# Optimization experiments

Hardware: AMD Instinct MI355X
Metric: run time of the kernel (lower is better)

The kernel has to match this reference:

```python
import jax, jax.numpy as jnp
import numpy as np
from jax.scipy.special import logsumexp

G, H, L, N, K = 2000, 128, 10, 4096, 10
TAU, LC, LA, EPS = 0.1, 1.0, 0.5, 1e-6

def _lin_init(k, fi, fo):
    return jax.random.normal(k, (fi, fo), jnp.float32) / np.sqrt(fi)

def setup_inputs():
    key = jax.random.key(0)
    ks = jax.random.split(key, 12)
    return {
        'wt_x': jax.random.normal(ks[0], (N, G), jnp.float32),
        'ko_x': jax.random.normal(ks[1], (N, G), jnp.float32),
        'wt_labels': jax.random.randint(ks[2], (N,), 0, K, dtype=jnp.int32),
        'ko_labels': jax.random.randint(ks[3], (N,), 0, K, dtype=jnp.int32),
        'enc_w1': _lin_init(ks[4], G, H), 'enc_b1': jnp.zeros((H,)),
        'enc_g': jnp.ones((H,)), 'enc_be': jnp.zeros((H,)),
        'enc_w2': _lin_init(ks[5], H, L), 'enc_b2': jnp.zeros((L,)),
        'kap_w1': _lin_init(ks[6], G, H), 'kap_b1': jnp.zeros((H,)),
        'kap_g': jnp.ones((H,)), 'kap_be': jnp.zeros((H,)),
        'kap_w2': _lin_init(ks[7], H, 1), 'kap_b2': jnp.zeros((1,)),
        'dec_w1': _lin_init(ks[8], L, H), 'dec_b1': jnp.zeros((H,)),
        'dec_g': jnp.ones((H,)), 'dec_be': jnp.zeros((H,)),
        'dec_w2': _lin_init(ks[9], H, G), 'dec_b2': jnp.zeros((G,)),
    }

def _mlp(x, w1, b1, g, be, w2, b2):
    # Linear -> LayerNorm -> ReLU -> Linear (dropout_prob=0)
    h = x @ w1 + b1
    m = h.mean(-1, keepdims=True)
    v = ((h - m) ** 2).mean(-1, keepdims=True)
    h = (h - m) / jnp.sqrt(v + 1e-5) * g + be
    return jax.nn.relu(h) @ w2 + b2

def _contrastive(z_wt, z_ko, y_wt, y_ko):
    S = (z_wt @ z_ko.T) / TAU  # [Nwt, Nko], unit-norm z so |S| <= 1/tau
    total = jnp.float32(0.0)
    n_shared = jnp.float32(0.0)
    for c in range(K):  # fixed small class count
        mwt = (y_wt == c).astype(S.dtype)
        mko = (y_ko == c).astype(S.dtype)
        n_wt, n_ko = mwt.sum(), mko.sum()
        valid = (n_wt > 0) & (n_ko > 0)
        nw, nk = jnp.maximum(n_wt, 1.0), jnp.maximum(n_ko, 1.0)
        # mean_{i in c, j in c} (LSE_i - S_ij) over ko columns of class c
        lse_r = logsumexp(jnp.where(mko[None, :] > 0, S, -1e4), axis=1)
        l1 = jnp.sum(mwt * (lse_r - (S @ mko) / nk)) / nw
        lse_c = logsumexp(jnp.where(mwt[:, None] > 0, S, -1e4), axis=0)
        l2 = jnp.sum(mko * (lse_c - (mwt @ S) / nw)) / nk
        total = total + jnp.where(valid, 0.5 * (l1 + l2), 0.0)
        n_shared = n_shared + valid.astype(S.dtype)
    return jnp.where(n_shared > 0, total / jnp.maximum(n_shared, 1.0), 0.0)

def _alignment(z, y):
    ones = jnp.ones(z.shape[0], z.dtype)
    counts = jax.ops.segment_sum(ones, y, num_segments=K)
    mu_c = jax.ops.segment_sum(z, y, num_segments=K) / jnp.maximum(counts, 1.0)[:, None]
    dev = z - mu_c[y]
    per_class = jax.ops.segment_sum(jnp.sum(dev ** 2, axis=1), y, num_segments=K) / jnp.maximum(counts, 1.0)
    present = counts > 0
    return jnp.sum(jnp.where(present, per_class, 0.0)) / jnp.maximum(jnp.sum(present.astype(z.dtype)), 1.0)

def reference(wt_x, ko_x, enc_w1, enc_b1, enc_g, enc_be, enc_w2, enc_b2, kap_w1, kap_b1, kap_g, kap_be, kap_w2, kap_b2, dec_w1, dec_b1, dec_g, dec_be, dec_w2, dec_b2, wt_labels, ko_labels):
    def encode(x):
        mu = _mlp(x, enc_w1, enc_b1, enc_g, enc_be, enc_w2, enc_b2)
        mu = mu / jnp.maximum(jnp.linalg.norm(mu, axis=1, keepdims=True), 1e-12)
        kappa = jax.nn.softplus(_mlp(x, kap_w1, kap_b1, kap_g, kap_be, kap_w2, kap_b2)) + EPS
        return mu, kappa
    wt_mu, wt_kappa = encode(wt_x)
    ko_mu, ko_kappa = encode(ko_x)
    wt_z, ko_z = wt_mu, ko_mu  # eval mode: z = mu (deterministic)
    wt_rec = _mlp(wt_z, dec_w1, dec_b1, dec_g, dec_be, dec_w2, dec_b2)
    ko_rec = _mlp(ko_z, dec_w1, dec_b1, dec_g, dec_be, dec_w2, dec_b2)
    recon = jnp.mean((wt_rec - wt_x) ** 2) + jnp.mean((ko_rec - ko_x) ** 2)
    kl = (wt_kappa.mean() + ko_kappa.mean()) * 0.01
    contrast = _contrastive(wt_z, ko_z, wt_labels, ko_labels)
    align = _alignment(jnp.concatenate([wt_z, ko_z], 0), jnp.concatenate([wt_labels, ko_labels], 0))
    return recon + kl + LC * contrast + LA * align
```

## Files before the change

### kernel.cpp

```cpp
#include <hip/hip_runtime.h>
#include <math.h>

typedef __attribute__((ext_vector_type(8))) __bf16 bf16x8;
typedef __attribute__((ext_vector_type(4))) float f32x4;

#define GL2LDS_(gptr, lptr) \
    __builtin_amdgcn_global_load_lds((const __attribute__((address_space(1))) void*)(gptr), \
                                     (__attribute__((address_space(3))) void*)(lptr), 16, 0, 0)

#define OFF_NWT   0
#define OFF_NKO   10
#define OFF_L1    20
#define OFF_L2    30
#define OFF_REC   162
#define IOFF_WTOFF 192
#define IOFF_KOOFF 204
#define IOFF_WTCTR 216
#define ACC_FLOATS 256

#define WT_OFF    256
#define WTLO_OFF  (WT_OFF + 262144)
#define H_OFF     (WTLO_OFF + 262144)
#define Z_OFF     (H_OFF + 2097152)
#define KAP_OFF   (Z_OFF + 81920)
#define HREST_OFF (KAP_OFF + 8192)
#define HPART     2097152

__global__ __launch_bounds__(256) void pack_w_kernel(const float* __restrict__ enc_w1,
                                                     const float* __restrict__ kap_w1,
                                                     __bf16* __restrict__ WThi,
                                                     __bf16* __restrict__ WTlo)
{
    __shared__ float tile[64][65];
    int kt = blockIdx.x & 31;
    int ct = blockIdx.x >> 5;
    int k0 = kt * 64, c0 = ct * 64;
    int t = threadIdx.x;
    int lr = t >> 6, lc = t & 63;
#pragma unroll
    for (int i = 0; i < 16; ++i) {
        int k = k0 + lr + 4 * i;
        int c = c0 + lc;
        float v = 0.f;
        if (k < 2000) v = (c < 128) ? enc_w1[(size_t)k * 128 + c]
                                    : kap_w1[(size_t)k * 128 + (c - 128)];
        tile[lc][lr + 4 * i] = v;
    }
    __syncthreads();
#pragma unroll
    for (int i = 0; i < 16; ++i) {
        int c = c0 + lr + 4 * i;
        int k = k0 + lc;
        float v = tile[lr + 4 * i][lc];
        __bf16 h = (__bf16)v;
        __bf16 l = (__bf16)(v - (float)h);
        size_t idx = (size_t)c * 2048 + k;
        WThi[idx] = h;
        WTlo[idx] = l;
    }
}

__global__ __launch_bounds__(256) void pack_dw2_kernel(const float* __restrict__ dw2,
                                                       __bf16* __restrict__ BThi,
                                                       __bf16* __restrict__ BTlo)
{
    __shared__ float tile[64][129];
    int j0 = blockIdx.x * 64;
    int t = threadIdx.x;
#pragma unroll
    for (int i = 0; i < 32; ++i) {
        int idx = i * 256 + t;
        int c = idx >> 6, jj = idx & 63;
        int j = j0 + jj;
        tile[jj][c] = (j < 2000) ? dw2[(size_t)c * 2000 + j] : 0.f;
    }
    __syncthreads();
#pragma unroll
    for (int i = 0; i < 32; ++i) {
        int idx = i * 256 + t;
        int jj = idx >> 7, c = idx & 127;
        float v = tile[jj][c];
        __bf16 h = (__bf16)v;
        size_t o = (size_t)(j0 + jj) * 128 + c;
        BThi[o] = h;
        BTlo[o] = (__bf16)(v - (float)h);
    }
}

__global__ void counts_kernel(const int* __restrict__ wtl, const int* __restrict__ kol,
                              float* __restrict__ acc)
{
    __shared__ int cw[10], ck[10];
    int t = threadIdx.x;
    if (t < 10) { cw[t] = 0; ck[t] = 0; }
    __syncthreads();
    for (int i = t; i < 4096; i += 1024) {
        atomicAdd(&cw[wtl[i]], 1);
        atomicAdd(&ck[kol[i]], 1);
    }
    __syncthreads();
    if (t < 10) { acc[OFF_NWT + t] = (float)cw[t]; acc[OFF_NKO + t] = (float)ck[t]; }
    if (t == 0) {
        int* ai = (int*)acc;
        int aw = 0, ak = 0;
        for (int c = 0; c < 10; ++c) {
            ai[IOFF_WTOFF + c] = aw; aw += cw[c];
            ai[IOFF_KOOFF + c] = ak; ak += ck[c];
        }
        ai[IOFF_WTOFF + 10] = aw;
        ai[IOFF_KOOFF + 10] = ak;
    }
}

__global__ __launch_bounds__(512) void gemm1_kernel(const float* __restrict__ wt_x,
                                                    const float* __restrict__ ko_x,
                                                    const __bf16* __restrict__ WThi,
                                                    const __bf16* __restrict__ WTlo,
                                                    float* __restrict__ Hb,
                                                    float* __restrict__ Hrest,
                                                    int nkc)
{
    __shared__ short Bs[2][2][2][4096];
    int t = threadIdx.x;
    int widx = t >> 6, lane = t & 63;
    int wm = widx >> 1, wn = widx & 1;
    int b = blockIdx.x;
    int mt = b & 63, strip = (b >> 6) & 1, kc = b >> 7;
    int R0 = mt * 128;
    int cb = strip * 128;
    int kchunk = 2048 / nkc;
    int kbase = kc * kchunk;
    int kleft = 2000 - kbase;
    int nsteps = (kleft < kchunk) ? ((kleft + 31) >> 5) : (kchunk >> 5);
    int ntiles = (nsteps + 1) >> 1;

    const float* xb = (R0 < 4096) ? (wt_x + (size_t)R0 * 2000)
                                  : (ko_x + (size_t)(R0 - 4096) * 2000);
    int ar = wm * 32 + (lane & 15);
    const float* xrow0 = xb + (size_t)ar * 2000 + kbase;
    const float* xrow1 = xrow0 + (size_t)16 * 2000;
    int kboff = (lane >> 4) * 8;

    int col0 = t >> 2;
    int s0   = (t & 3) ^ ((col0 >> 1) & 3);
    size_t boff = (size_t)(cb + col0) * 2048 + kbase + s0 * 8;
    const __bf16* bsrcH = WThi + boff;
    const __bf16* bsrcL = WTlo + boff;

#define STAGEB_(buf, tl) do { \
    int st_ = (tl) * 2; \
    GL2LDS_(bsrcH + (size_t)st_ * 32,       &Bs[buf][0][0][t * 8]); \
    GL2LDS_(bsrcH + (size_t)(st_ + 1) * 32, &Bs[buf][0][1][t * 8]); \
    GL2LDS_(bsrcL + (size_t)st_ * 32,       &Bs[buf][1][0][t * 8]); \
    GL2LDS_(bsrcL + (size_t)(st_ + 1) * 32, &Bs[buf][1][1][t * 8]); } while (0)

    f32x4 acc00, acc01, acc02, acc03;
    f32x4 acc10, acc11, acc12, acc13;
#pragma unroll
    for (int r = 0; r < 4; ++r) {
        acc00[r]=0.f; acc01[r]=0.f; acc02[r]=0.f; acc03[r]=0.f;
        acc10[r]=0.f; acc11[r]=0.f; acc12[r]=0.f; acc13[r]=0.f;
    }

    float4 aA00, aA01, aA10, aA11, aA20, aA21, aA30, aA31;
    float4 aB00, aB01, aB10, aB11, aB20, aB21, aB30, aB31;

#define GLOADA_(step, a00, a01, a10, a11) do { \
    int k0_ = (step) * 32; \
    int k_ = k0_ + kboff; \
    if (kbase + k0_ <= 1952) { \
        a00 = *(const float4*)(xrow0 + k_); \
        a01 = *(const float4*)(xrow0 + k_ + 4); \
        a10 = *(const float4*)(xrow1 + k_); \
        a11 = *(const float4*)(xrow1 + k_ + 4); \
    } else { \
        float t0_[8], t1_[8]; \
        _Pragma("unroll") \
        for (int j = 0; j < 8; ++j) { \
            int kk = kbase + k_ + j; \
            t0_[j] = (kk < 2000) ? xrow0[k_ + j] : 0.f; \
            t1_[j] = (kk < 2000) ? xrow1[k_ + j] : 0.f; } \
        a00 = make_float4(t0_[0], t0_[1], t0_[2], t0_[3]); \
        a01 = make_float4(t0_[4], t0_[5], t0_[6], t0_[7]); \
        a10 = make_float4(t1_[0], t1_[1], t1_[2], t1_[3]); \
        a11 = make_float4(t1_[4], t1_[5], t1_[6], t1_[7]); } } while (0)

#define CONVA_(a0, a1, ahi, alo) do { \
    float av_[8] = {a0.x, a0.y, a0.z, a0.w, a1.x, a1.y, a1.z, a1.w}; \
    _Pragma("unroll") \
    for (int j = 0; j < 8; ++j) { \
        __bf16 h_ = (__bf16)av_[j]; \
        ahi[j] = h_; \
        alo[j] = (__bf16)(av_[j] - (float)h_); } } while (0)

#define MFMAH_(buf, half, ahi0, alo0, ahi1, alo1) do { \
    _Pragma("unroll") \
    for (int nf = 0; nf < 4; ++nf) { \
        bf16x8 bhf = *(const bf16x8*)&Bs[buf][0][half][(ubase + nf * 64) * 8]; \
        bf16x8 blf = *(const bf16x8*)&Bs[buf][1][half][(ubase + nf * 64) * 8]; \
        f32x4* p0 = (nf == 0) ? &acc00 : (nf == 1) ? &acc01 : (nf == 2) ? &acc02 : &acc03; \
        f32x4* p1 = (nf == 0) ? &acc10 : (nf == 1) ? &acc11 : (nf == 2) ? &acc12 : &acc13; \
        *p0 = __builtin_amdgcn_mfma_f32_16x16x32_bf16(ahi0, bhf, *p0, 0, 0, 0); \
        *p0 = __builtin_amdgcn_mfma_f32_16x16x32_bf16(alo0, bhf, *p0, 0, 0, 0); \
        *p0 = __builtin_amdgcn_mfma_f32_16x16x32_bf16(ahi0, blf, *p0, 0, 0, 0); \
        *p1 = __builtin_amdgcn_mfma_f32_16x16x32_bf16(ahi1, bhf, *p1, 0, 0, 0); \
        *p1 = __builtin_amdgcn_mfma_f32_16x16x32_bf16(alo1, bhf, *p1, 0, 0, 0); \
        *p1 = __builtin_amdgcn_mfma_f32_16x16x32_bf16(ahi1, blf, *p1, 0, 0, 0); } } while (0)

    STAGEB_(0, 0);
    GLOADA_(0, aA00, aA01, aA10, aA11);
    GLOADA_(1, aA20, aA21, aA30, aA31);
    if (1 < ntiles) {
        GLOADA_(2, aB00, aB01, aB10, aB11);
        GLOADA_(3, aB20, aB21, aB30, aB31);
    }
    __syncthreads();

    int cpr = lane & 15;
    int pph = (lane >> 4) ^ ((cpr >> 1) & 3);
    int ubase = (wn * 64 + cpr) * 4 + pph;

    int half_iters = (ntiles + 1) >> 1;
    for (int it = 0; it < half_iters; ++it) {
        int tl = it * 2;
        {
            if (tl + 1 < ntiles) STAGEB_(1, tl + 1);
            bf16x8 h00,l00,h01,l01,h10,l10,h11,l11;
            CONVA_(aA00, aA01, h00, l00); CONVA_(aA10, aA11, h01, l01);
            CONVA_(aA20, aA21, h10, l10); CONVA_(aA30, aA31, h11, l11);
            if (tl + 2 < ntiles) {
                GLOADA_(2*(tl+2),   aA00, aA01, aA10, aA11);
                GLOADA_(2*(tl+2)+1, aA20, aA21, aA30, aA31);
            }
            MFMAH_(0, 0, h00, l00, h01, l01);
            MFMAH_(0, 1, h10, l10, h11, l11);
            __syncthreads();
        }
        if (tl + 1 < ntiles) {
            if (tl + 2 < ntiles) STAGEB_(0, tl + 2);
            bf16x8 h00,l00,h01,l01,h10,l10,h11,l11;
            CONVA_(aB00, aB01, h00, l00); CONVA_(aB10, aB11, h01, l01);
            CONVA_(aB20, aB21, h10, l10); CONVA_(aB30, aB31, h11, l11);
            if (tl + 3 < ntiles) {
                GLOADA_(2*(tl+3),   aB00, aB01, aB10, aB11);
                GLOADA_(2*(tl+3)+1, aB20, aB21, aB30, aB31);
            }
            MFMAH_(1, 0, h00, l00, h01, l01);
            MFMAH_(1, 1, h10, l10, h11, l11);
            __syncthreads();
        }
    }

    float* Hq = (kc == 0) ? Hb : (Hrest + (size_t)(kc - 1) * HPART);
#pragma unroll
    for (int r = 0; r < 4; ++r) {
        int row0 = R0 + wm * 32 + (lane >> 4) * 4 + r;
        size_t base0 = (size_t)row0 * 256 + cb + wn * 64 + (lane & 15);
        Hq[base0]      = acc00[r];
        Hq[base0 + 16] = acc01[r];
        Hq[base0 + 32] = acc02[r];
        Hq[base0 + 48] = acc03[r];
        size_t base1 = base0 + (size_t)16 * 256;
        Hq[base1]      = acc10[r];
        Hq[base1 + 16] = acc11[r];
        Hq[base1 + 32] = acc12[r];
        Hq[base1 + 48] = acc13[r];
    }
#undef STAGEB_
#undef GLOADA_
#undef CONVA_
#undef MFMAH_
}

__global__ __launch_bounds__(128) void stage2_kernel(const float* __restrict__ Hb,
    const float* __restrict__ Hrest, int nkc,
    const float* __restrict__ enc_b1, const float* __restrict__ enc_g, const float* __restrict__ enc_be,
    const float* __restrict__ enc_w2, const float* __restrict__ enc_b2,
    const float* __restrict__ kap_b1, const float* __restrict__ kap_g, const float* __restrict__ kap_be,
    const float* __restrict__ kap_w2, const float* __restrict__ kap_b2,
    const float* __restrict__ dw1, const float* __restrict__ db1,
    const float* __restrict__ dg,  const float* __restrict__ dbe,
    float* __restrict__ Z, float* __restrict__ Kap,
    __bf16* __restrict__ Ahi, __bf16* __restrict__ Alo)
{
    __shared__ float sh[128];
    __shared__ float shz[10];
    __shared__ float dred[2], dvar[2];
    int row  = blockIdx.x;
    int wave = threadIdx.x >> 6;
    int lane = threadIdx.x & 63;
    size_t hoff = (size_t)row * 256 + wave * 128;
    const float* hb  = Hb + hoff;
    const float* b1 = wave ? kap_b1 : enc_b1;
    const float* gg = wave ? kap_g  : enc_g;
    const float* bb = wave ? kap_be : enc_be;

    float h0 = hb[lane]      + b1[lane];
    float h1 = hb[lane + 64] + b1[lane + 64];
    for (int j = 0; j + 1 < nkc; ++j) {
        const float* hr = Hrest + (size_t)j * HPART + hoff;
        h0 += hr[lane];
        h1 += hr[lane + 64];
    }
    float s = h0 + h1;
#pragma unroll
    for (int o = 32; o > 0; o >>= 1) s += __shfl_xor(s, o, 64);
    float m = s * (1.f / 128.f);
    float d0 = h0 - m, d1 = h1 - m;
    float v = d0 * d0 + d1 * d1;
#pragma unroll
    for (int o = 32; o > 0; o >>= 1) v += __shfl_xor(v, o, 64);
    v *= (1.f / 128.f);
    float sc = 1.f / sqrtf(v + 1e-5f);
    float r0 = fmaxf(fmaf(d0 * sc, gg[lane],      bb[lane]),      0.f);
    float r1 = fmaxf(fmaf(d1 * sc, gg[lane + 64], bb[lane + 64]), 0.f);

    if (wave == 0) { sh[lane] = r0; sh[lane + 64] = r1; }
    __syncthreads();

    if (wave == 0) {
        float mu = 0.f;
        if (lane < 10) {
            mu = enc_b2[lane];
            for (int c = 0; c < 128; ++c) mu = fmaf(sh[c], enc_w2[c * 10 + lane], mu);
        }
        float n2 = mu * mu;
#pragma unroll
        for (int o = 8; o > 0; o >>= 1) n2 += __shfl_xor(n2, o, 16);
        float inv = 1.f / fmaxf(sqrtf(n2), 1e-12f);
        if (lane < 10) {
            float zv = mu * inv;
            Z[(size_t)row * 10 + lane] = zv;
            shz[lane] = zv;
        }
    } else {
        float p = r0 * kap_w2[lane] + r1 * kap_w2[lane + 64];
#pragma unroll
        for (int o = 32; o > 0; o >>= 1) p += __shfl_xor(p, o, 64);
        if (lane == 0) {
            float x = p + kap_b2[0];
            float sp = (x > 20.f) ? x : log1pf(expf(x));
            Kap[row] = sp + 1e-6f;
        }
    }
    __syncthreads();

    {
        float z[10];
#pragma unroll
        for (int d = 0; d < 10; ++d) z[d] = shz[d];
        int c = threadIdx.x;
        float h = db1[c];
#pragma unroll
        for (int d = 0; d < 10; ++d) h = fmaf(z[d], dw1[d * 128 + c], h);
        float s2 = h;
#pragma unroll
        for (int o = 32; o > 0; o >>= 1) s2 += __shfl_xor(s2, o, 64);
        if (lane == 0) dred[wave] = s2;
        __syncthreads();
        float m2 = (dred[0] + dred[1]) * (1.f / 128.f);
        float dd = h - m2;
        float v2 = dd * dd;
#pragma unroll
        for (int o = 32; o > 0; o >>= 1) v2 += __shfl_xor(v2, o, 64);
        if (lane == 0) dvar[wave] = v2;
        __syncthreads();
        float var = (dvar[0] + dvar[1]) * (1.f / 128.f);
        float sc2 = 1.f / sqrtf(var + 1e-5f);
        float a = fmaxf(fmaf(dd * sc2, dg[c], dbe[c]), 0.f);
        __bf16 hb_ = (__bf16)a;
        size_t base = (size_t)row * 128 + c;
        Ahi[base] = hb_;
        Alo[base] = (__bf16)(a - (float)hb_);
    }
}

__global__ __launch_bounds__(256) void scatter_align_kernel(const float* __restrict__ Z,
                                                            const int* __restrict__ wtl,
                                                            const int* __restrict__ kol,
                                                            const float* __restrict__ Kap,
                                                            float* __restrict__ acc,
                                                            float* __restrict__ ZcWT,
                                                            float* __restrict__ ZcKO,
                                                            float* __restrict__ Part)
{
    __shared__ int lcnt[20];
    __shared__ int lbase[20];
    __shared__ float cL[10], qL[10], sL[100], ks;
    int t = threadIdx.x;
    if (t < 20) lcnt[t] = 0;
    if (t < 10) { cL[t] = 0.f; qL[t] = 0.f; }
    if (t >= 20 && t < 120) sL[t - 20] = 0.f;
    if (t == 120) ks = 0.f;
    __syncthreads();
    int row = blockIdx.x * 256 + t;
    int side = row >= 4096;
    int r = side ? row - 4096 : row;
    int c = side ? kol[r] : wtl[r];
    int key = side * 10 + c;
    int myrank = atomicAdd(&lcnt[key], 1);
    float zz[10]; float q = 0.f;
    const float* zr = Z + (size_t)row * 10;
#pragma unroll
    for (int d = 0; d < 10; ++d) { zz[d] = zr[d]; q = fmaf(zz[d], zz[d], q); }
    atomicAdd(&cL[c], 1.f);
    atomicAdd(&qL[c], q);
#pragma unroll
    for (int d = 0; d < 10; ++d) atomicAdd(&sL[c * 10 + d], zz[d]);
    atomicAdd(&ks, Kap[row]);
    __syncthreads();
    int* ai = (int*)acc;
    if (t < 20 && lcnt[t] > 0)
        lbase[t] = atomicAdd(&ai[IOFF_WTCTR + t], lcnt[t]);
    __syncthreads();
    int off = side ? ai[IOFF_KOOFF + c] : ai[IOFF_WTOFF + c];
    int slot = off + lbase[key] + myrank;
    float* dst = side ? ZcKO : ZcWT;
#pragma unroll
    for (int d = 0; d < 10; ++d) dst[d * 4096 + slot] = zz[d];
    float* pb = Part + (size_t)blockIdx.x * 128;
    if (t < 10)  { pb[t] = cL[t]; pb[10 + t] = qL[t]; }
    if (t < 100) pb[20 + t] = sL[t];
    if (t == 0)  pb[120] = ks;
}

__global__ __launch_bounds__(512, 4) void dec_gemm_kernel(
    const __bf16* __restrict__ Ahi, const __bf16* __restrict__ Alo,
    const __bf16* __restrict__ BThi, const __bf16* __restrict__ BTlo,
    const float* __restrict__ wt_x, const float* __restrict__ ko_x,
    const float* __restrict__ db2, float* __restrict__ acc)
{
    __shared__ short BsH[2][8192];
    __shared__ short BsL[2][8192];
    __shared__ float rs[8];
    int t = threadIdx.x;
    int widx = t >> 6, lane = t & 63;
    int wm = widx >> 2, wn = widx & 3;
    int R0 = (blockIdx.x >> 1) * 32;
    int T0 = (blockIdx.x & 1) * 16;
    const float* xbase = (R0 < 4096) ? wt_x : ko_x;
    int xr0 = ((R0 < 4096) ? R0 : R0 - 4096) + wm * 16 + (lane >> 4) * 4;

    size_t abase = (size_t)(R0 + wm * 16 + (lane & 15)) * 128 + (lane >> 4) * 8;
    bf16x8 ah0 = *(const bf16x8*)(Ahi + abase);
    bf16x8 ah1 = *(const bf16x8*)(Ahi + abase + 32);
    bf16x8 ah2 = *(const bf16x8*)(Ahi + abase + 64);
    bf16x8 ah3 = *(const bf16x8*)(Ahi + abase + 96);
    bf16x8 al0 = *(const bf16x8*)(Alo + abase);
    bf16x8 al1 = *(const bf16x8*)(Alo + abase + 32);
    bf16x8 al2 = *(const bf16x8*)(Alo + abase + 64);
    bf16x8 al3 = *(const bf16x8*)(Alo + abase + 96);

    int g0c = t >> 4,         g0s = t & 15;
    int g1c = (t + 512) >> 4, g1s = t & 15;
    int u0 = g0c * 16 + (g0s ^ (g0c & 7));
    int u1 = g1c * 16 + (g1s ^ (g1c & 7));

    int col_local = wn * 16 + (lane & 15);
    int cl7 = col_local & 7;
    int rb = col_local * 16;
    int sb = lane >> 4;

    uint4 hA0, hA1, lA0, lA1, hB0, hB1, lB0, lB1;

#define GLOADB_(tile, h0, h1, l0, l1) do { \
    size_t gb = (size_t)(tile) * 8192; \
    h0 = *(const uint4*)(BThi + gb + (size_t)t * 8); \
    h1 = *(const uint4*)(BThi + gb + (size_t)(t + 512) * 8); \
    l0 = *(const uint4*)(BTlo + gb + (size_t)t * 8); \
    l1 = *(const uint4*)(BTlo + gb + (size_t)(t + 512) * 8); } while (0)

#define DSWRITE_(buf, h0, h1, l0, l1) do { \
    *(uint4*)&BsH[buf][u0 * 8] = h0; \
    *(uint4*)&BsH[buf][u1 * 8] = h1; \
    *(uint4*)&BsL[buf][u0 * 8] = l0; \
    *(uint4*)&BsL[buf][u1 * 8] = l1; } while (0)

#define COMPUTE_(buf, tile) do { \
    int un0 = rb + ((sb +  0) ^ cl7); \
    int un1 = rb + ((sb +  4) ^ cl7); \
    int un2 = rb + ((sb +  8) ^ cl7); \
    int un3 = rb + ((sb + 12) ^ cl7); \
    bf16x8 bh0 = *(const bf16x8*)&BsH[buf][un0 * 8]; \
    bf16x8 bh1 = *(const bf16x8*)&BsH[buf][un1 * 8]; \
    bf16x8 bh2 = *(const bf16x8*)&BsH[buf][un2 * 8]; \
    bf16x8 bh3 = *(const bf16x8*)&BsH[buf][un3 * 8]; \
    bf16x8 bl0 = *(const bf16x8*)&BsL[buf][un0 * 8]; \
    bf16x8 bl1 = *(const bf16x8*)&BsL[buf][un1 * 8]; \
    bf16x8 bl2 = *(const bf16x8*)&BsL[buf][un2 * 8]; \
    bf16x8 bl3 = *(const bf16x8*)&BsL[buf][un3 * 8]; \
    f32x4 a4; \
    _Pragma("unroll") \
    for (int r = 0; r < 4; ++r) a4[r] = 0.f; \
    a4 = __builtin_amdgcn_mfma_f32_16x16x32_bf16(ah0, bh0, a4, 0, 0, 0); \
    a4 = __builtin_amdgcn_mfma_f32_16x16x32_bf16(al0, bh0, a4, 0, 0, 0); \
    a4 = __builtin_amdgcn_mfma_f32_16x16x32_bf16(ah0, bl0, a4, 0, 0, 0); \
    a4 = __builtin_amdgcn_mfma_f32_16x16x32_bf16(ah1, bh1, a4, 0, 0, 0); \
    a4 = __builtin_amdgcn_mfma_f32_16x16x32_bf16(al1, bh1, a4, 0, 0, 0); \
    a4 = __builtin_amdgcn_mfma_f32_16x16x32_bf16(ah1, bl1, a4, 0, 0, 0); \
    a4 = __builtin_amdgcn_mfma_f32_16x16x32_bf16(ah2, bh2, a4, 0, 0, 0); \
    a4 = __builtin_amdgcn_mfma_f32_16x16x32_bf16(al2, bh2, a4, 0, 0, 0); \
    a4 = __builtin_amdgcn_mfma_f32_16x16x32_bf16(ah2, bl2, a4, 0, 0, 0); \
    a4 = __builtin_amdgcn_mfma_f32_16x16x32_bf16(ah3, bh3, a4, 0, 0, 0); \
    a4 = __builtin_amdgcn_mfma_f32_16x16x32_bf16(al3, bh3, a4, 0, 0, 0); \
    a4 = __builtin_amdgcn_mfma_f32_16x16x32_bf16(ah3, bl3, a4, 0, 0, 0); \
    int col = (tile) * 64 + col_local; \
    if (col < 2000) { \
        float bb = db2[col]; \
        _Pragma("unroll") \
        for (int r = 0; r < 4; ++r) { \
            float xv = xbase[(size_t)(xr0 + r) * 2000 + col]; \
            float e = a4[r] + bb - xv; \
            rsum = fmaf(e, e, rsum); \
        } } } while (0)

    float rsum = 0.f;
    GLOADB_(T0 + 0, hA0, hA1, lA0, lA1);
    GLOADB_(T0 + 1, hB0, hB1, lB0, lB1);
    DSWRITE_(0, hA0, hA1, lA0, lA1);
    __syncthreads();

    for (int it = 0; it < 8; ++it) {
        int lt = it * 2;
        {
            if (lt + 2 < 16) GLOADB_(T0 + lt + 2, hA0, hA1, lA0, lA1);
            DSWRITE_(1, hB0, hB1, lB0, lB1);
            COMPUTE_(0, T0 + lt);
            __syncthreads();
        }
        {
            if (lt + 3 < 16) GLOADB_(T0 + lt + 3, hB0, hB1, lB0, lB1);
            if (lt + 2 < 16) DSWRITE_(0, hA0, hA1, lA0, lA1);
            COMPUTE_(1, T0 + lt + 1);
            __syncthreads();
        }
    }

#pragma unroll
    for (int o = 32; o > 0; o >>= 1) rsum += __shfl_xor(rsum, o, 64);
    if (lane == 0) rs[widx] = rsum;
    __syncthreads();
    if (t == 0) {
        float s = 0.f;
#pragma unroll
        for (int w = 0; w < 8; ++w) s += rs[w];
        atomicAdd(&acc[OFF_REC], s);
    }
#undef GLOADB_
#undef DSWRITE_
#undef COMPUTE_
}

#define MAXNB 768
__global__ __launch_bounds__(256) void contrast_kernel(const float* __restrict__ ZcWT,
                                                       const float* __restrict__ ZcKO,
                                                       float* __restrict__ acc)
{
    __shared__ float zb[MAXNB * 12];
    __shared__ float bsum[4];
    int b = blockIdx.x;
    int cs = b / 3, sub = b - cs * 3;
    int c = cs >> 1, side = cs & 1;
    const int* ai = (const int*)acc;
    int aStart = side ? ai[IOFF_KOOFF + c]     : ai[IOFF_WTOFF + c];
    int aEnd   = side ? ai[IOFF_KOOFF + c + 1] : ai[IOFF_WTOFF + c + 1];
    int bStart = side ? ai[IOFF_WTOFF + c]     : ai[IOFF_KOOFF + c];
    int bEnd   = side ? ai[IOFF_WTOFF + c + 1] : ai[IOFF_KOOFF + c + 1];
    int na = aEnd - aStart;
    int nb = bEnd - bStart;
    if (nb > MAXNB) nb = MAXNB;
    const float* ZA = side ? ZcKO : ZcWT;
    const float* ZB = side ? ZcWT : ZcKO;
    int t = threadIdx.x;

    for (int u = t; u < nb; u += 256) {
#pragma unroll
        for (int d = 0; d < 10; ++d) zb[u * 12 + d] = ZB[d * 4096 + bStart + u];
    }
    __syncthreads();

    int chunk = (na + 2) / 3;
    int r0 = sub * chunk;
    int rcnt = na - r0; if (rcnt > chunk) rcnt = chunk;

    float wsum = 0.f;
    bool waveActive = (nb > 0) && ((t & ~63) < rcnt);
    if (waveActive) {
        bool valid = t < rcnt;
        int ar = aStart + (valid ? (r0 + t) : 0);
        float za[10];
#pragma unroll
        for (int d = 0; d < 10; ++d) za[d] = ZA[d * 4096 + ar];
        float se = 0.f, ss = 0.f;
        for (int u = 0; u < nb; ++u) {
            const float* zp = &zb[u * 12];
            float s = 0.f;
#pragma unroll
            for (int d = 0; d < 10; ++d) s = fmaf(za[d], zp[d], s);
            s *= 10.f;
            se += __expf(s - 10.f);
            ss += s;
        }
        if (valid) wsum = (10.f + __logf(se)) - ss / (float)nb;
    }
#pragma unroll
    for (int o = 32; o > 0; o >>= 1) wsum += __shfl_xor(wsum, o, 64);
    if ((t & 63) == 0) bsum[t >> 6] = wsum;
    __syncthreads();
    if (t == 0) {
        float s = bsum[0] + bsum[1] + bsum[2] + bsum[3];
        if (s != 0.f || nb > 0)
            atomicAdd(&acc[(side ? OFF_L2 : OFF_L1) + c], s);
    }
}

__global__ void finalize_kernel(const float* __restrict__ Part,
                                const float* __restrict__ acc,
                                float* __restrict__ out)
{
    __shared__ float red[121];
    int t = threadIdx.x;
    if (t < 120) {
        float s = 0.f;
        for (int b = 0; b < 32; ++b) s += Part[(size_t)b * 128 + t];
        red[t] = s;
    } else if (t == 120) {
        float s = 0.f;
        for (int b = 0; b < 32; ++b) s += Part[(size_t)b * 128 + 120];
        red[120] = s;
    }
    __syncthreads();
    if (t == 0) {
        float total = 0.f, nsh = 0.f;
        for (int c = 0; c < 10; ++c) {
            float nw = acc[OFF_NWT + c], nk = acc[OFF_NKO + c];
            if (nw > 0.5f && nk > 0.5f) {
                float l1 = acc[OFF_L1 + c] / nw;
                float l2 = acc[OFF_L2 + c] / nk;
                total += 0.5f * (l1 + l2);
                nsh += 1.f;
            }
        }
        float contrast = (nsh > 0.f) ? total / nsh : 0.f;
        float ap = 0.f, np_ = 0.f;
        for (int c = 0; c < 10; ++c) {
            float cn = red[c];
            if (cn > 0.5f) {
                float mu2 = 0.f;
                for (int d = 0; d < 10; ++d) {
                    float mm = red[20 + c * 10 + d] / cn;
                    mu2 = fmaf(mm, mm, mu2);
                }
                ap += red[10 + c] / cn - mu2;
                np_ += 1.f;
            }
        }
        float align = (np_ > 0.f) ? ap / np_ : 0.f;
        float kl = 0.01f * red[120] * (1.f / 4096.f);
        float recon = acc[OFF_REC] * (1.f / 8192000.f);
        out[0] = recon + kl + 1.0f * contrast + 0.5f * align;
    }
}

extern "C" void kernel_launch(void* const* d_in, const int* in_sizes, int n_in,
                              void* d_out, int out_size, void* d_ws, size_t ws_size,
                              hipStream_t stream)
{
    const float* wt_x   = (const float*)d_in[0];
    const float* ko_x   = (const float*)d_in[1];
    const int*   wtl    = (const int*)d_in[2];
    const int*   kol    = (const int*)d_in[3];
    const float* enc_w1 = (const float*)d_in[4];
    const float* enc_b1 = (const float*)d_in[5];
    const float* enc_g  = (const float*)d_in[6];
    const float* enc_be = (const float*)d_in[7];
    const float* enc_w2 = (const float*)d_in[8];
    const float* enc_b2 = (const float*)d_in[9];
    const float* kap_w1 = (const float*)d_in[10];
    const float* kap_b1 = (const float*)d_in[11];
    const float* kap_g  = (const float*)d_in[12];
    const float* kap_be = (const float*)d_in[13];
    const float* kap_w2 = (const float*)d_in[14];
    const float* kap_b2 = (const float*)d_in[15];
    const float* dw1    = (const float*)d_in[16];
    const float* db1    = (const float*)d_in[17];
    const float* dg     = (const float*)d_in[18];
    const float* dbe    = (const float*)d_in[19];
    const float* dw2    = (const float*)d_in[20];
    const float* db2    = (const float*)d_in[21];

    float* ws  = (float*)d_ws;
    float* acc = ws;
    __bf16* WThi = (__bf16*)(ws + WT_OFF);
    __bf16* WTlo = (__bf16*)(ws + WTLO_OFF);
    float* Hb    = ws + H_OFF;
    float* Zb    = ws + Z_OFF;
    float* Kap   = ws + KAP_OFF;
    float* Hrest = ws + HREST_OFF;

    const size_t TAIL = 2 * 524288 + 2 * 131072 + 2 * 40960 + 4096;
    size_t need4 = (size_t)(HREST_OFF + 3 * HPART + TAIL) * sizeof(float);
    int nkc = (ws_size >= need4) ? 4 : 2;

    float* tail = ws + HREST_OFF + (size_t)(nkc - 1) * HPART;
    __bf16* Ahi  = (__bf16*)tail;
    __bf16* Alo  = (__bf16*)(tail + 524288);
    __bf16* BThi = (__bf16*)(tail + 1048576);
    __bf16* BTlo = (__bf16*)(tail + 1048576 + 131072);
    float* ZcKO = tail + 1048576 + 262144;
    float* ZcWT = ZcKO + 40960;
    float* Part = ZcWT + 40960;

    hipMemsetAsync(acc, 0, ACC_FLOATS * sizeof(float), stream);
    pack_w_kernel<<<128, 256, 0, stream>>>(enc_w1, kap_w1, WThi, WTlo);
    counts_kernel<<<1, 1024, 0, stream>>>(wtl, kol, acc);
    gemm1_kernel<<<128 * nkc, 512, 0, stream>>>(wt_x, ko_x, WThi, WTlo, Hb, Hrest, nkc);
    stage2_kernel<<<8192, 128, 0, stream>>>(Hb, Hrest, nkc, enc_b1, enc_g, enc_be, enc_w2, enc_b2,
                                            kap_b1, kap_g, kap_be, kap_w2, kap_b2,
                                            dw1, db1, dg, dbe, Zb, Kap, Ahi, Alo);
    pack_dw2_kernel<<<32, 256, 0, stream>>>(dw2, BThi, BTlo);
    scatter_align_kernel<<<32, 256, 0, stream>>>(Zb, wtl, kol, Kap, acc, ZcWT, ZcKO, Part);
    contrast_kernel<<<60, 256, 0, stream>>>(ZcWT, ZcKO, acc);
    dec_gemm_kernel<<<512, 512, 0, stream>>>(Ahi, Alo, BThi, BTlo, wt_x, ko_x, db2, acc);
    finalize_kernel<<<1, 128, 0, stream>>>(Part, acc, (float*)d_out);
}
```

Before: 171.4 us.

## Double gemm1 row tile to 256 and stage one k-step of B per buffer

The encoder first-layer GEMM now gives each block 256 rows instead of 128, so each warp computes 64 rows with 16 accumulators. Each staged B tile is reused across twice as many rows, halving B traffic and the block count. The LDS buffer shrinks to one 32-wide k-step per stage, which doubles the number of barriers per k. Register pressure rises, and with only 64*nkc blocks (256 at nkc=4) occupancy and load balance on a 256-CU part may suffer.

```diff
diff --git a/kernel.cpp b/kernel.cpp
--- a/kernel.cpp
+++ b/kernel.cpp
@@ -120,25 +120,26 @@
                                                     float* __restrict__ Hrest,
                                                     int nkc)
 {
-    __shared__ short Bs[2][2][2][4096];
+    __shared__ short Bs[2][2][4096];
     int t = threadIdx.x;
     int widx = t >> 6, lane = t & 63;
     int wm = widx >> 1, wn = widx & 1;
     int b = blockIdx.x;
-    int mt = b & 63, strip = (b >> 6) & 1, kc = b >> 7;
-    int R0 = mt * 128;
+    int mt = b & 31, strip = (b >> 5) & 1, kc = b >> 6;
+    int R0 = mt * 256;
     int cb = strip * 128;
     int kchunk = 2048 / nkc;
     int kbase = kc * kchunk;
     int kleft = 2000 - kbase;
     int nsteps = (kleft < kchunk) ? ((kleft + 31) >> 5) : (kchunk >> 5);
-    int ntiles = (nsteps + 1) >> 1;
 
     const float* xb = (R0 < 4096) ? (wt_x + (size_t)R0 * 2000)
                                   : (ko_x + (size_t)(R0 - 4096) * 2000);
-    int ar = wm * 32 + (lane & 15);
+    int ar = wm * 64 + (lane & 15);
     const float* xrow0 = xb + (size_t)ar * 2000 + kbase;
     const float* xrow1 = xrow0 + (size_t)16 * 2000;
+    const float* xrow2 = xrow0 + (size_t)32 * 2000;
+    const float* xrow3 = xrow0 + (size_t)48 * 2000;
     int kboff = (lane >> 4) * 8;
 
     int col0 = t >> 2;
@@ -147,43 +148,45 @@
     const __bf16* bsrcH = WThi + boff;
     const __bf16* bsrcL = WTlo + boff;
 
-#define STAGEB_(buf, tl) do { \
-    int st_ = (tl) * 2; \
-    GL2LDS_(bsrcH + (size_t)st_ * 32,       &Bs[buf][0][0][t * 8]); \
-    GL2LDS_(bsrcH + (size_t)(st_ + 1) * 32, &Bs[buf][0][1][t * 8]); \
-    GL2LDS_(bsrcL + (size_t)st_ * 32,       &Bs[buf][1][0][t * 8]); \
-    GL2LDS_(bsrcL + (size_t)(st_ + 1) * 32, &Bs[buf][1][1][t * 8]); } while (0)
+#define STAGEB_(buf, step) do { \
+    GL2LDS_(bsrcH + (size_t)(step) * 32, &Bs[buf][0][t * 8]); \
+    GL2LDS_(bsrcL + (size_t)(step) * 32, &Bs[buf][1][t * 8]); } while (0)
 
     f32x4 acc00, acc01, acc02, acc03;
     f32x4 acc10, acc11, acc12, acc13;
+    f32x4 acc20, acc21, acc22, acc23;
+    f32x4 acc30, acc31, acc32, acc33;
 #pragma unroll
     for (int r = 0; r < 4; ++r) {
         acc00[r]=0.f; acc01[r]=0.f; acc02[r]=0.f; acc03[r]=0.f;
         acc10[r]=0.f; acc11[r]=0.f; acc12[r]=0.f; acc13[r]=0.f;
-    }
-
-    float4 aA00, aA01, aA10, aA11, aA20, aA21, aA30, aA31;
-    float4 aB00, aB01, aB10, aB11, aB20, aB21, aB30, aB31;
-
-#define GLOADA_(step, a00, a01, a10, a11) do { \
+        acc20[r]=0.f; acc21[r]=0.f; acc22[r]=0.f; acc23[r]=0.f;
+        acc30[r]=0.f; acc31[r]=0.f; acc32[r]=0.f; acc33[r]=0.f;
+    }
+
+    float4 aA00,aA01, aA10,aA11, aA20,aA21, aA30,aA31;
+    float4 aB00,aB01, aB10,aB11, aB20,aB21, aB30,aB31;
+
+#define GLOAD1_(xrw, step, a0, a1) do { \
     int k0_ = (step) * 32; \
     int k_ = k0_ + kboff; \
     if (kbase + k0_ <= 1952) { \
-        a00 = *(const float4*)(xrow0 + k_); \
-        a01 = *(const float4*)(xrow0 + k_ + 4); \
-        a10 = *(const float4*)(xrow1 + k_); \
-        a11 = *(const float4*)(xrow1 + k_ + 4); \
+        a0 = *(const float4*)((xrw) + k_); \
+        a1 = *(const float4*)((xrw) + k_ + 4); \
     } else { \
-        float t0_[8], t1_[8]; \
+        float t_[8]; \
         _Pragma("unroll") \
         for (int j = 0; j < 8; ++j) { \
             int kk = kbase + k_ + j; \
-            t0_[j] = (kk < 2000) ? xrow0[k_ + j] : 0.f; \
-            t1_[j] = (kk < 2000) ? xrow1[k_ + j] : 0.f; } \
-        a00 = make_float4(t0_[0], t0_[1], t0_[2], t0_[3]); \
-        a01 = make_float4(t0_[4], t0_[5], t0_[6], t0_[7]); \
-        a10 = make_float4(t1_[0], t1_[1], t1_[2], t1_[3]); \
-        a11 = make_float4(t1_[4], t1_[5], t1_[6], t1_[7]); } } while (0)
+            t_[j] = (kk < 2000) ? (xrw)[k_ + j] : 0.f; } \
+        a0 = make_float4(t_[0], t_[1], t_[2], t_[3]); \
+        a1 = make_float4(t_[4], t_[5], t_[6], t_[7]); } } while (0)
+
+#define GLOADA4_(step, s0a,s0b, s1a,s1b, s2a,s2b, s3a,s3b) do { \
+    GLOAD1_(xrow0, step, s0a, s0b); \
+    GLOAD1_(xrow1, step, s1a, s1b); \
+    GLOAD1_(xrow2, step, s2a, s2b); \
+    GLOAD1_(xrow3, step, s3a, s3b); } while (0)
 
 #define CONVA_(a0, a1, ahi, alo) do { \
     float av_[8] = {a0.x, a0.y, a0.z, a0.w, a1.x, a1.y, a1.z, a1.w}; \
@@ -193,60 +196,60 @@
         ahi[j] = h_; \
         alo[j] = (__bf16)(av_[j] - (float)h_); } } while (0)
 
-#define MFMAH_(buf, half, ahi0, alo0, ahi1, alo1) do { \
+#define MFMASTEP_(buf, h0,l0, h1,l1, h2,l2, h3,l3) do { \
     _Pragma("unroll") \
     for (int nf = 0; nf < 4; ++nf) { \
-        bf16x8 bhf = *(const bf16x8*)&Bs[buf][0][half][(ubase + nf * 64) * 8]; \
-        bf16x8 blf = *(const bf16x8*)&Bs[buf][1][half][(ubase + nf * 64) * 8]; \
+        bf16x8 bhf = *(const bf16x8*)&Bs[buf][0][(ubase + nf * 64) * 8]; \
+        bf16x8 blf = *(const bf16x8*)&Bs[buf][1][(ubase + nf * 64) * 8]; \
         f32x4* p0 = (nf == 0) ? &acc00 : (nf == 1) ? &acc01 : (nf == 2) ? &acc02 : &acc03; \
         f32x4* p1 = (nf == 0) ? &acc10 : (nf == 1) ? &acc11 : (nf == 2) ? &acc12 : &acc13; \
-        *p0 = __builtin_amdgcn_mfma_f32_16x16x32_bf16(ahi0, bhf, *p0, 0, 0, 0); \
-        *p0 = __builtin_amdgcn_mfma_f32_16x16x32_bf16(alo0, bhf, *p0, 0, 0, 0); \
-        *p0 = __builtin_amdgcn_mfma_f32_16x16x32_bf16(ahi0, blf, *p0, 0, 0, 0); \
-        *p1 = __builtin_amdgcn_mfma_f32_16x16x32_bf16(ahi1, bhf, *p1, 0, 0, 0); \
-        *p1 = __builtin_amdgcn_mfma_f32_16x16x32_bf16(alo1, bhf, *p1, 0, 0, 0); \
-        *p1 = __builtin_amdgcn_mfma_f32_16x16x32_bf16(ahi1, blf, *p1, 0, 0, 0); } } while (0)
+        f32x4* p2 = (nf == 0) ? &acc20 : (nf == 1) ? &acc21 : (nf == 2) ? &acc22 : &acc23; \
+        f32x4* p3 = (nf == 0) ? &acc30 : (nf == 1) ? &acc31 : (nf == 2) ? &acc32 : &acc33; \
+        *p0 = __builtin_amdgcn_mfma_f32_16x16x32_bf16(h0, bhf, *p0, 0, 0, 0); \
+        *p0 = __builtin_amdgcn_mfma_f32_16x16x32_bf16(l0, bhf, *p0, 0, 0, 0); \
+        *p0 = __builtin_amdgcn_mfma_f32_16x16x32_bf16(h0, blf, *p0, 0, 0, 0); \
+        *p1 = __builtin_amdgcn_mfma_f32_16x16x32_bf16(h1, bhf, *p1, 0, 0, 0); \
+        *p1 = __builtin_amdgcn_mfma_f32_16x16x32_bf16(l1, bhf, *p1, 0, 0, 0); \
+        *p1 = __builtin_amdgcn_mfma_f32_16x16x32_bf16(h1, blf, *p1, 0, 0, 0); \
+        *p2 = __builtin_amdgcn_mfma_f32_16x16x32_bf16(h2, bhf, *p2, 0, 0, 0); \
+        *p2 = __builtin_amdgcn_mfma_f32_16x16x32_bf16(l2, bhf, *p2, 0, 0, 0); \
+        *p2 = __builtin_amdgcn_mfma_f32_16x16x32_bf16(h2, blf, *p2, 0, 0, 0); \
+        *p3 = __builtin_amdgcn_mfma_f32_16x16x32_bf16(h3, bhf, *p3, 0, 0, 0); \
+        *p3 = __builtin_amdgcn_mfma_f32_16x16x32_bf16(l3, bhf, *p3, 0, 0, 0); \
+        *p3 = __builtin_amdgcn_mfma_f32_16x16x32_bf16(h3, blf, *p3, 0, 0, 0); } } while (0)
 
     STAGEB_(0, 0);
-    GLOADA_(0, aA00, aA01, aA10, aA11);
-    GLOADA_(1, aA20, aA21, aA30, aA31);
-    if (1 < ntiles) {
-        GLOADA_(2, aB00, aB01, aB10, aB11);
-        GLOADA_(3, aB20, aB21, aB30, aB31);
-    }
+    GLOADA4_(0, aA00,aA01, aA10,aA11, aA20,aA21, aA30,aA31);
+    if (1 < nsteps) GLOADA4_(1, aB00,aB01, aB10,aB11, aB20,aB21, aB30,aB31);
     __syncthreads();
 
     int cpr = lane & 15;
     int pph = (lane >> 4) ^ ((cpr >> 1) & 3);
     int ubase = (wn * 64 + cpr) * 4 + pph;
 
-    int half_iters = (ntiles + 1) >> 1;
-    for (int it = 0; it < half_iters; ++it) {
-        int tl = it * 2;
+    int niter = (nsteps + 1) >> 1;
+    for (int it = 0; it < niter; ++it) {
+        int st0 = it * 2;
         {
-            if (tl + 1 < ntiles) STAGEB_(1, tl + 1);
-            bf16x8 h00,l00,h01,l01,h10,l10,h11,l11;
-            CONVA_(aA00, aA01, h00, l00); CONVA_(aA10, aA11, h01, l01);
-            CONVA_(aA20, aA21, h10, l10); CONVA_(aA30, aA31, h11, l11);
-            if (tl + 2 < ntiles) {
-                GLOADA_(2*(tl+2),   aA00, aA01, aA10, aA11);
-                GLOADA_(2*(tl+2)+1, aA20, aA21, aA30, aA31);
-            }
-            MFMAH_(0, 0, h00, l00, h01, l01);
-            MFMAH_(0, 1, h10, l10, h11, l11);
+            if (st0 + 1 < nsteps) STAGEB_(1, st0 + 1);
+            bf16x8 h0,l0,h1,l1,h2,l2,h3,l3;
+            CONVA_(aA00, aA01, h0, l0);
+            CONVA_(aA10, aA11, h1, l1);
+            CONVA_(aA20, aA21, h2, l2);
+            CONVA_(aA30, aA31, h3, l3);
+            if (st0 + 2 < nsteps) GLOADA4_(st0 + 2, aA00,aA01, aA10,aA11, aA20,aA21, aA30,aA31);
+            MFMASTEP_(0, h0,l0, h1,l1, h2,l2, h3,l3);
             __syncthreads();
         }
-        if (tl + 1 < ntiles) {
-            if (tl + 2 < ntiles) STAGEB_(0, tl + 2);
-            bf16x8 h00,l00,h01,l01,h10,l10,h11,l11;
-            CONVA_(aB00, aB01, h00, l00); CONVA_(aB10, aB11, h01, l01);
-            CONVA_(aB20, aB21, h10, l10); CONVA_(aB30, aB31, h11, l11);
-            if (tl + 3 < ntiles) {
-                GLOADA_(2*(tl+3),   aB00, aB01, aB10, aB11);
-                GLOADA_(2*(tl+3)+1, aB20, aB21, aB30, aB31);
-            }
-            MFMAH_(1, 0, h00, l00, h01, l01);
-            MFMAH_(1, 1, h10, l10, h11, l11);
+        if (st0 + 1 < nsteps) {
+            if (st0 + 2 < nsteps) STAGEB_(0, st0 + 2);
+            bf16x8 h0,l0,h1,l1,h2,l2,h3,l3;
+            CONVA_(aB00, aB01, h0, l0);
+            CONVA_(aB10, aB11, h1, l1);
+            CONVA_(aB20, aB21, h2, l2);
+            CONVA_(aB30, aB31, h3, l3);
+            if (st0 + 3 < nsteps) GLOADA4_(st0 + 3, aB00,aB01, aB10,aB11, aB20,aB21, aB30,aB31);
+            MFMASTEP_(1, h0,l0, h1,l1, h2,l2, h3,l3);
             __syncthreads();
         }
     }
@@ -254,22 +257,22 @@
     float* Hq = (kc == 0) ? Hb : (Hrest + (size_t)(kc - 1) * HPART);
 #pragma unroll
     for (int r = 0; r < 4; ++r) {
-        int row0 = R0 + wm * 32 + (lane >> 4) * 4 + r;
-        size_t base0 = (size_t)row0 * 256 + cb + wn * 64 + (lane & 15);
-        Hq[base0]      = acc00[r];
-        Hq[base0 + 16] = acc01[r];
-        Hq[base0 + 32] = acc02[r];
-        Hq[base0 + 48] = acc03[r];
-        size_t base1 = base0 + (size_t)16 * 256;
-        Hq[base1]      = acc10[r];
-        Hq[base1 + 16] = acc11[r];
-        Hq[base1 + 32] = acc12[r];
-        Hq[base1 + 48] = acc13[r];
+        int rowb = R0 + wm * 64 + (lane >> 4) * 4 + r;
+        size_t cbase = cb + wn * 64 + (lane & 15);
+        size_t b0 = (size_t)(rowb +  0) * 256 + cbase;
+        size_t b1 = (size_t)(rowb + 16) * 256 + cbase;
+        size_t b2 = (size_t)(rowb + 32) * 256 + cbase;
+        size_t b3 = (size_t)(rowb + 48) * 256 + cbase;
+        Hq[b0] = acc00[r]; Hq[b0+16] = acc01[r]; Hq[b0+32] = acc02[r]; Hq[b0+48] = acc03[r];
+        Hq[b1] = acc10[r]; Hq[b1+16] = acc11[r]; Hq[b1+32] = acc12[r]; Hq[b1+48] = acc13[r];
+        Hq[b2] = acc20[r]; Hq[b2+16] = acc21[r]; Hq[b2+32] = acc22[r]; Hq[b2+48] = acc23[r];
+        Hq[b3] = acc30[r]; Hq[b3+16] = acc31[r]; Hq[b3+32] = acc32[r]; Hq[b3+48] = acc33[r];
     }
 #undef STAGEB_
-#undef GLOADA_
+#undef GLOAD1_
+#undef GLOADA4_
 #undef CONVA_
-#undef MFMAH_
+#undef MFMASTEP_
 }
 
 __global__ __launch_bounds__(128) void stage2_kernel(const float* __restrict__ Hb,
@@ -714,7 +717,7 @@
     hipMemsetAsync(acc, 0, ACC_FLOATS * sizeof(float), stream);
     pack_w_kernel<<<128, 256, 0, stream>>>(enc_w1, kap_w1, WThi, WTlo);
     counts_kernel<<<1, 1024, 0, stream>>>(wtl, kol, acc);
-    gemm1_kernel<<<128 * nkc, 512, 0, stream>>>(wt_x, ko_x, WThi, WTlo, Hb, Hrest, nkc);
+    gemm1_kernel<<<64 * nkc, 512, 0, stream>>>(wt_x, ko_x, WThi, WTlo, Hb, Hrest, nkc);
     stage2_kernel<<<8192, 128, 0, stream>>>(Hb, Hrest, nkc, enc_b1, enc_g, enc_be, enc_w2, enc_b2,
                                             kap_b1, kap_g, kap_be, kap_w2, kap_b2,
                                             dw1, db1, dg, dbe, Zb, Kap, Ahi, Alo);
```

Result: slower. 182.6 us (+6.5%).
